# Optimization experiments

Hardware: AMD Instinct MI355X
Metric: run time of the kernel (lower is better)

The kernel has to match this reference:

```python
import jax, jax.numpy as jnp
import numpy as np
import math

S, D = 8192, 128

def setup_inputs() -> dict:
    key = jax.random.key(0)
    kq, kk, kv = jax.random.split(key, 3)
    return {
        "q": jax.random.normal(kq, (S, D), dtype=jnp.float32),
        "k": jax.random.normal(kk, (S, D), dtype=jnp.float32),
        "v": jax.random.normal(kv, (S, D), dtype=jnp.float32),
    }

def reference(q, k, v):
    # scores: [S, S]; scale by sqrt(d) as in the torch module
    scale = 1.0 / math.sqrt(q.shape[1])
    scores = (q @ k.T) * scale
    attn = jax.nn.softmax(scores, axis=-1)
    return attn @ v
```

## Files before the change

### kernel.cpp

```cpp
#include <hip/hip_runtime.h>
#include <hip/hip_bf16.h>

#define SEQ 8192
#define HD 128
#define BM 256
#define BN 64
#define NQT (SEQ / BM)
#define THREADS 512

typedef __bf16 bf16_t;
typedef __bf16 bf16x2 __attribute__((ext_vector_type(2)));
typedef __bf16 bf16x8 __attribute__((ext_vector_type(8)));
typedef float f32x4 __attribute__((ext_vector_type(4)));
typedef float f32x16 __attribute__((ext_vector_type(16)));
typedef unsigned int u32x4 __attribute__((ext_vector_type(4)));

#if __has_builtin(__builtin_amdgcn_exp2f)
__device__ inline float exp2_fast(float x) { return __builtin_amdgcn_exp2f(x); }
#else
__device__ inline float exp2_fast(float x) { return exp2f(x); }
#endif

__device__ inline void permswap32(unsigned int& a, unsigned int& b) {
#if __has_builtin(__builtin_amdgcn_permlane32_swap)
  auto r = __builtin_amdgcn_permlane32_swap(a, b, false, false);
  a = (unsigned int)r[0];
  b = (unsigned int)r[1];
#else
  asm volatile("v_permlane32_swap_b32 %0, %1" : "+v"(a), "+v"(b));
#endif
}

__device__ inline void load_lds16(const void* g, void* l) {
  __builtin_amdgcn_global_load_lds(
      (const __attribute__((address_space(1))) void*)g,
      (__attribute__((address_space(3))) void*)l, 16, 0, 0);
}

__global__ __launch_bounds__(256) void prep_kernel(const float* __restrict__ K,
                                                   const float* __restrict__ V,
                                                   bf16_t* __restrict__ Kb,
                                                   bf16_t* __restrict__ VT) {
  const int b = (int)blockIdx.x;
  const int tid = (int)threadIdx.x;
  if (b < 256) {
    __shared__ float tile[64][65];
    const int T = b & 127;
    const int d0 = (b >> 7) * 64;
    const int s0 = T * 64;
    const int r = tid >> 2;
    const int c0 = (tid & 3) * 16;
#pragma unroll
    for (int j4 = 0; j4 < 4; ++j4) {
      float4 x = *(const float4*)&V[(size_t)(s0 + r) * HD + d0 + c0 + j4 * 4];
      tile[r][c0 + j4 * 4 + 0] = x.x;
      tile[r][c0 + j4 * 4 + 1] = x.y;
      tile[r][c0 + j4 * 4 + 2] = x.z;
      tile[r][c0 + j4 * 4 + 3] = x.w;
    }
    __syncthreads();
    const int d_l = tid & 63;
    const int kc0 = (tid >> 6) * 2;
#pragma unroll
    for (int k2 = 0; k2 < 2; ++k2) {
      const int kc = kc0 + k2;
      bf16x8 wv;
#pragma unroll
      for (int j = 0; j < 8; ++j) wv[j] = (bf16_t)tile[kc * 8 + j][d_l];
      *(bf16x8*)&VT[((size_t)(T * 8 + kc) * 128 + d0 + d_l) * 8] = wv;
    }
  } else {
    const int base = (b - 256) * 2048 + tid * 8;
    const int row = base >> 7;
    const int c = (base >> 3) & 15;
    const int T = row >> 6;
    const int r = row & 63;
    float4 a = *(const float4*)&K[base];
    float4 cc = *(const float4*)&K[base + 4];
    bf16x8 f;
    f[0] = (bf16_t)a.x; f[1] = (bf16_t)a.y; f[2] = (bf16_t)a.z; f[3] = (bf16_t)a.w;
    f[4] = (bf16_t)cc.x; f[5] = (bf16_t)cc.y; f[6] = (bf16_t)cc.z; f[7] = (bf16_t)cc.w;
    *(bf16x8*)&Kb[((size_t)(T * 16 + c) * 64 + r) * 8] = f;
  }
}

__global__ __launch_bounds__(THREADS, 2) void fattn_kernel(
    const float* __restrict__ Q, const bf16_t* __restrict__ Kb,
    const bf16_t* __restrict__ VT, float* __restrict__ Opart,
    float* __restrict__ Lpart, int kshift, int nit) {
  __shared__ __align__(16) bf16_t kt2[2][16][64][8];
  __shared__ __align__(16) bf16_t vt3[3][8][128][8];

  const int tid = (int)threadIdx.x;
  const int lane = tid & 63;
  const int w = tid >> 6;
  const int h = lane >> 5;
  const int n32 = lane & 31;

  const int qt = (int)blockIdx.x >> kshift;
  const int sp = (int)blockIdx.x & ((1 << kshift) - 1);
  const int qbase = qt * BM;
  const int tile0 = sp * nit;

  const float SC2 = 0.08838834764831845f * 1.4426950408889634f;

  bf16x8 qf[8];
  {
    const float* qp = Q + (size_t)(qbase + w * 32 + n32) * HD + h * 8;
#pragma unroll
    for (int kk = 0; kk < 8; ++kk) {
      float4 a = *(const float4*)(qp + kk * 16);
      float4 b = *(const float4*)(qp + kk * 16 + 4);
      bf16x8 f;
      f[0] = (bf16_t)(a.x * SC2); f[1] = (bf16_t)(a.y * SC2);
      f[2] = (bf16_t)(a.z * SC2); f[3] = (bf16_t)(a.w * SC2);
      f[4] = (bf16_t)(b.x * SC2); f[5] = (bf16_t)(b.y * SC2);
      f[6] = (bf16_t)(b.z * SC2); f[7] = (bf16_t)(b.w * SC2);
      qf[kk] = f;
    }
  }

  f32x16 o_acc[4];
#pragma unroll
  for (int i = 0; i < 4; ++i)
#pragma unroll
    for (int e = 0; e < 16; ++e) o_acc[i][e] = 0.f;
  float l_acc = 0.f;

  bf16x8 paA[4], paB[4];

  const int rr0 = w * 2;

#define EXPPACK1(SACC, KK2, PDST_EXPR)                                     \
  {                                                                        \
    float pf[8];                                                           \
    _Pragma("unroll")                                                      \
    for (int j = 0; j < 8; ++j) pf[j] = exp2_fast((SACC)[8 * (KK2) + j]);  \
    l_acc += ((pf[0] + pf[1]) + (pf[2] + pf[3])) +                         \
             ((pf[4] + pf[5]) + (pf[6] + pf[7]));                          \
    bf16x2 p0, p1, p2, p3;                                                 \
    p0[0] = (bf16_t)pf[0]; p0[1] = (bf16_t)pf[1];                          \
    p1[0] = (bf16_t)pf[2]; p1[1] = (bf16_t)pf[3];                          \
    p2[0] = (bf16_t)pf[4]; p2[1] = (bf16_t)pf[5];                          \
    p3[0] = (bf16_t)pf[6]; p3[1] = (bf16_t)pf[7];                          \
    unsigned int sA = __builtin_bit_cast(unsigned int, p0);                \
    unsigned int sB = __builtin_bit_cast(unsigned int, p1);                \
    unsigned int sC = __builtin_bit_cast(unsigned int, p2);                \
    unsigned int sD = __builtin_bit_cast(unsigned int, p3);                \
    permswap32(sA, sC);                                                    \
    permswap32(sB, sD);                                                    \
    u32x4 fv;                                                              \
    fv[0] = sA; fv[1] = sB; fv[2] = sC; fv[3] = sD;                        \
    (PDST_EXPR) = __builtin_bit_cast(bf16x8, fv);                          \
  }

#define PVC(PP, C)                                                         \
  _Pragma("unroll")                                                        \
  for (int ot = 0; ot < 4; ++ot) {                                         \
    bf16x8 vb = *(const bf16x8*)&vt3[vp][(C) * 2 + h][ot * 32 + n32][0];   \
    o_acc[ot] = __builtin_amdgcn_mfma_f32_32x32x16_bf16(PP[C], vb, o_acc[ot], 0, 0, 0); \
  }

#define FBODY(IT, PPREV, PCUR, KC)                                         \
  {                                                                        \
    const int it_ = (IT);                                                  \
    if (it_ + 1 < nit) {                                                   \
      const int ntile = tile0 + it_ + 1;                                   \
      _Pragma("unroll")                                                    \
      for (int t = 0; t < 2; ++t) {                                        \
        const int rr = rr0 + t;                                            \
        load_lds16(Kb + ((size_t)(ntile * 16 + rr) * 64 + lane) * 8,       \
                   (char*)&kt2[(KC) ^ 1][0][0][0] + rr * 1024);            \
        load_lds16(VT + ((size_t)(ntile * 8 + (rr >> 1)) * 128 + (rr & 1) * 64 + lane) * 8, \
                   (char*)&vt3[vd][0][0][0] + rr * 1024);                  \
      }                                                                    \
    }                                                                      \
    f32x16 sacc0, sacc1;                                                   \
    _Pragma("unroll")                                                      \
    for (int e = 0; e < 16; ++e) { sacc0[e] = 0.f; sacc1[e] = 0.f; }       \
    _Pragma("unroll")                                                      \
    for (int kk = 0; kk < 8; ++kk) {                                       \
      bf16x8 af0 = *(const bf16x8*)&kt2[KC][2 * kk + h][n32][0];           \
      sacc0 = __builtin_amdgcn_mfma_f32_32x32x16_bf16(af0, qf[kk], sacc0, 0, 0, 0); \
      bf16x8 af1 = *(const bf16x8*)&kt2[KC][2 * kk + h][32 + n32][0];      \
      sacc1 = __builtin_amdgcn_mfma_f32_32x32x16_bf16(af1, qf[kk], sacc1, 0, 0, 0); \
    }                                                                      \
    PVC(PPREV, 0) EXPPACK1(sacc0, 0, PCUR[0])                              \
    PVC(PPREV, 1) EXPPACK1(sacc0, 1, PCUR[1])                              \
    PVC(PPREV, 2) EXPPACK1(sacc1, 0, PCUR[2])                              \
    PVC(PPREV, 3) EXPPACK1(sacc1, 1, PCUR[3])                              \
    vp = (vp + 1 == 3) ? 0 : vp + 1;                                       \
    vd = (vd + 1 == 3) ? 0 : vd + 1;                                       \
    __syncthreads();                                                       \
  }

#pragma unroll
  for (int t = 0; t < 2; ++t) {
    const int rr = rr0 + t;
    load_lds16(Kb + ((size_t)(tile0 * 16 + rr) * 64 + lane) * 8,
               (char*)&kt2[0][0][0][0] + rr * 1024);
    load_lds16(VT + ((size_t)(tile0 * 8 + (rr >> 1)) * 128 + (rr & 1) * 64 + lane) * 8,
               (char*)&vt3[0][0][0][0] + rr * 1024);
  }
  __syncthreads();

  {
    if (nit > 1) {
      const int ntile = tile0 + 1;
#pragma unroll
      for (int t = 0; t < 2; ++t) {
        const int rr = rr0 + t;
        load_lds16(Kb + ((size_t)(ntile * 16 + rr) * 64 + lane) * 8,
                   (char*)&kt2[1][0][0][0] + rr * 1024);
        load_lds16(VT + ((size_t)(ntile * 8 + (rr >> 1)) * 128 + (rr & 1) * 64 + lane) * 8,
                   (char*)&vt3[1][0][0][0] + rr * 1024);
      }
    }
    f32x16 sacc0, sacc1;
#pragma unroll
    for (int e = 0; e < 16; ++e) { sacc0[e] = 0.f; sacc1[e] = 0.f; }
#pragma unroll
    for (int kk = 0; kk < 8; ++kk) {
      bf16x8 af0 = *(const bf16x8*)&kt2[0][2 * kk + h][n32][0];
      sacc0 = __builtin_amdgcn_mfma_f32_32x32x16_bf16(af0, qf[kk], sacc0, 0, 0, 0);
      bf16x8 af1 = *(const bf16x8*)&kt2[0][2 * kk + h][32 + n32][0];
      sacc1 = __builtin_amdgcn_mfma_f32_32x32x16_bf16(af1, qf[kk], sacc1, 0, 0, 0);
    }
    EXPPACK1(sacc0, 0, paA[0])
    EXPPACK1(sacc0, 1, paA[1])
    EXPPACK1(sacc1, 0, paA[2])
    EXPPACK1(sacc1, 1, paA[3])
    __syncthreads();
  }

  int vp = 0;
  int vd = 2;

  for (int it = 1; it + 1 <= nit - 1; it += 2) {
    FBODY(it, paA, paB, 1)
    FBODY(it + 1, paB, paA, 0)
  }
  FBODY(nit - 1, paA, paB, 1)

#pragma unroll
  for (int C = 0; C < 4; ++C) {
#pragma unroll
    for (int ot = 0; ot < 4; ++ot) {
      bf16x8 vb = *(const bf16x8*)&vt3[vp][C * 2 + h][ot * 32 + n32][0];
      o_acc[ot] = __builtin_amdgcn_mfma_f32_32x32x16_bf16(paB[C], vb, o_acc[ot], 0, 0, 0);
    }
  }

#undef FBODY
#undef PVC
#undef EXPPACK1

  {
    float* op = Opart + ((size_t)sp * SEQ + qbase + w * 32) * HD;
#pragma unroll
    for (int ot = 0; ot < 4; ++ot)
#pragma unroll
      for (int reg = 0; reg < 16; ++reg) {
        const int row = (reg & 3) + 8 * (reg >> 2) + 4 * h;
        op[row * HD + ot * 32 + n32] = o_acc[ot][reg];
      }
    float l = l_acc + __shfl_xor(l_acc, 32);
    if (lane < 32)
      Lpart[(size_t)sp * SEQ + qbase + w * 32 + n32] = l;
  }
}

__global__ __launch_bounds__(256) void combine_kernel(const float* __restrict__ Opart,
                                                      const float* __restrict__ Lpart,
                                                      float* __restrict__ out, int ksplit) {
  const int tid = (int)threadIdx.x;
  const int row = (int)blockIdx.x * 8 + (tid >> 5);
  const int c0 = (tid & 31) * 4;
  float lsum = 0.f;
  for (int s = 0; s < ksplit; ++s) lsum += Lpart[(size_t)s * SEQ + row];
  f32x4 acc;
#pragma unroll
  for (int e = 0; e < 4; ++e) acc[e] = 0.f;
  for (int s = 0; s < ksplit; ++s) {
    f32x4 o = *(const f32x4*)&Opart[((size_t)s * SEQ + row) * HD + c0];
#pragma unroll
    for (int e = 0; e < 4; ++e) acc[e] += o[e];
  }
  const float inv = 1.0f / lsum;
  f32x4 res;
#pragma unroll
  for (int e = 0; e < 4; ++e) res[e] = acc[e] * inv;
  *(f32x4*)&out[(size_t)row * HD + c0] = res;
}

extern "C" void kernel_launch(void* const* d_in, const int* in_sizes, int n_in,
                              void* d_out, int out_size, void* d_ws, size_t ws_size,
                              hipStream_t stream) {
  const float* Q = (const float*)d_in[0];
  const float* K = (const float*)d_in[1];
  const float* V = (const float*)d_in[2];
  float* out = (float*)d_out;

  int ksplit = 8, kshift = 3;
  while (ksplit > 1) {
    size_t need = (size_t)ksplit * SEQ * HD * 4
                + (size_t)ksplit * SEQ * 4
                + (size_t)SEQ * HD * 2 * 2;
    if (need <= ws_size) break;
    ksplit >>= 1; kshift--;
  }

  char* ws = (char*)d_ws;
  float* Opart = (float*)ws;
  float* Lpart = (float*)(ws + (size_t)ksplit * SEQ * HD * 4);
  bf16_t* Kb = (bf16_t*)(ws + (size_t)ksplit * SEQ * HD * 4 + (size_t)ksplit * SEQ * 4);
  bf16_t* VT = Kb + (size_t)SEQ * HD;

  const int nit = SEQ / (ksplit * BN);

  prep_kernel<<<768, 256, 0, stream>>>(K, V, Kb, VT);
  fattn_kernel<<<NQT * ksplit, THREADS, 0, stream>>>(Q, Kb, VT, Opart, Lpart, kshift, nit);
  combine_kernel<<<SEQ / 8, 256, 0, stream>>>(Opart, Lpart, out, ksplit);
}
```

Baseline: 110.8 us.

## Halve attention block threads, each wave computes 64 query rows

Cuts the attention block from 8 waves to 4, and each wave now handles two 32-row query groups. Every K and V fragment read from LDS is therefore reused across two sets of MFMAs, which halves LDS read traffic per FLOP, and each thread issues twice as many async tile loads. The cost is doubled accumulator and Q-fragment registers per thread, with launch bounds relaxed to one block per CU, so occupancy drops and there is a risk of register spills or less latency hiding.

```diff
diff --git a/kernel.cpp b/kernel.cpp
--- a/kernel.cpp
+++ b/kernel.cpp
@@ -6,7 +6,7 @@
 #define BM 256
 #define BN 64
 #define NQT (SEQ / BM)
-#define THREADS 512
+#define THREADS 256
 
 typedef __bf16 bf16_t;
 typedef __bf16 bf16x2 __attribute__((ext_vector_type(2)));
@@ -84,7 +84,7 @@
   }
 }
 
-__global__ __launch_bounds__(THREADS, 2) void fattn_kernel(
+__global__ __launch_bounds__(THREADS, 1) void fattn_kernel(
     const float* __restrict__ Q, const bf16_t* __restrict__ Kb,
     const bf16_t* __restrict__ VT, float* __restrict__ Opart,
     float* __restrict__ Lpart, int kshift, int nit) {
@@ -104,9 +104,10 @@
 
   const float SC2 = 0.08838834764831845f * 1.4426950408889634f;
 
-  bf16x8 qf[8];
-  {
-    const float* qp = Q + (size_t)(qbase + w * 32 + n32) * HD + h * 8;
+  bf16x8 qf[2][8];
+#pragma unroll
+  for (int qg = 0; qg < 2; ++qg) {
+    const float* qp = Q + (size_t)(qbase + w * 64 + qg * 32 + n32) * HD + h * 8;
 #pragma unroll
     for (int kk = 0; kk < 8; ++kk) {
       float4 a = *(const float4*)(qp + kk * 16);
@@ -116,28 +117,30 @@
       f[2] = (bf16_t)(a.z * SC2); f[3] = (bf16_t)(a.w * SC2);
       f[4] = (bf16_t)(b.x * SC2); f[5] = (bf16_t)(b.y * SC2);
       f[6] = (bf16_t)(b.z * SC2); f[7] = (bf16_t)(b.w * SC2);
-      qf[kk] = f;
-    }
-  }
-
-  f32x16 o_acc[4];
-#pragma unroll
-  for (int i = 0; i < 4; ++i)
-#pragma unroll
-    for (int e = 0; e < 16; ++e) o_acc[i][e] = 0.f;
-  float l_acc = 0.f;
-
-  bf16x8 paA[4], paB[4];
-
-  const int rr0 = w * 2;
-
-#define EXPPACK1(SACC, KK2, PDST_EXPR)                                     \
+      qf[qg][kk] = f;
+    }
+  }
+
+  f32x16 o_acc[2][4];
+#pragma unroll
+  for (int qg = 0; qg < 2; ++qg)
+#pragma unroll
+    for (int i = 0; i < 4; ++i)
+#pragma unroll
+      for (int e = 0; e < 16; ++e) o_acc[qg][i][e] = 0.f;
+  float l_acc0 = 0.f, l_acc1 = 0.f;
+
+  bf16x8 paA[2][4], paB[2][4];
+
+  const int rr0 = w * 4;
+
+#define EXPPACK1(SACC, KK2, PDST_EXPR, LACC)                               \
   {                                                                        \
     float pf[8];                                                           \
     _Pragma("unroll")                                                      \
     for (int j = 0; j < 8; ++j) pf[j] = exp2_fast((SACC)[8 * (KK2) + j]);  \
-    l_acc += ((pf[0] + pf[1]) + (pf[2] + pf[3])) +                         \
-             ((pf[4] + pf[5]) + (pf[6] + pf[7]));                          \
+    LACC += ((pf[0] + pf[1]) + (pf[2] + pf[3])) +                          \
+            ((pf[4] + pf[5]) + (pf[6] + pf[7]));                           \
     bf16x2 p0, p1, p2, p3;                                                 \
     p0[0] = (bf16_t)pf[0]; p0[1] = (bf16_t)pf[1];                          \
     p1[0] = (bf16_t)pf[2]; p1[1] = (bf16_t)pf[3];                          \
@@ -154,11 +157,12 @@
     (PDST_EXPR) = __builtin_bit_cast(bf16x8, fv);                          \
   }
 
-#define PVC(PP, C)                                                         \
+#define PVC2(PP, C)                                                        \
   _Pragma("unroll")                                                        \
   for (int ot = 0; ot < 4; ++ot) {                                         \
     bf16x8 vb = *(const bf16x8*)&vt3[vp][(C) * 2 + h][ot * 32 + n32][0];   \
-    o_acc[ot] = __builtin_amdgcn_mfma_f32_32x32x16_bf16(PP[C], vb, o_acc[ot], 0, 0, 0); \
+    o_acc[0][ot] = __builtin_amdgcn_mfma_f32_32x32x16_bf16(PP[0][C], vb, o_acc[0][ot], 0, 0, 0); \
+    o_acc[1][ot] = __builtin_amdgcn_mfma_f32_32x32x16_bf16(PP[1][C], vb, o_acc[1][ot], 0, 0, 0); \
   }
 
 #define FBODY(IT, PPREV, PCUR, KC)                                         \
@@ -167,7 +171,7 @@
     if (it_ + 1 < nit) {                                                   \
       const int ntile = tile0 + it_ + 1;                                   \
       _Pragma("unroll")                                                    \
-      for (int t = 0; t < 2; ++t) {                                        \
+      for (int t = 0; t < 4; ++t) {                                        \
         const int rr = rr0 + t;                                            \
         load_lds16(Kb + ((size_t)(ntile * 16 + rr) * 64 + lane) * 8,       \
                    (char*)&kt2[(KC) ^ 1][0][0][0] + rr * 1024);            \
@@ -175,27 +179,33 @@
                    (char*)&vt3[vd][0][0][0] + rr * 1024);                  \
       }                                                                    \
     }                                                                      \
-    f32x16 sacc0, sacc1;                                                   \
+    f32x16 s00, s10, s01, s11;        \
     _Pragma("unroll")                                                      \
-    for (int e = 0; e < 16; ++e) { sacc0[e] = 0.f; sacc1[e] = 0.f; }       \
+    for (int e = 0; e < 16; ++e) { s00[e] = 0.f; s10[e] = 0.f; s01[e] = 0.f; s11[e] = 0.f; } \
     _Pragma("unroll")                                                      \
     for (int kk = 0; kk < 8; ++kk) {                                       \
       bf16x8 af0 = *(const bf16x8*)&kt2[KC][2 * kk + h][n32][0];           \
-      sacc0 = __builtin_amdgcn_mfma_f32_32x32x16_bf16(af0, qf[kk], sacc0, 0, 0, 0); \
       bf16x8 af1 = *(const bf16x8*)&kt2[KC][2 * kk + h][32 + n32][0];      \
-      sacc1 = __builtin_amdgcn_mfma_f32_32x32x16_bf16(af1, qf[kk], sacc1, 0, 0, 0); \
+      s00 = __builtin_amdgcn_mfma_f32_32x32x16_bf16(af0, qf[0][kk], s00, 0, 0, 0); \
+      s10 = __builtin_amdgcn_mfma_f32_32x32x16_bf16(af1, qf[0][kk], s10, 0, 0, 0); \
+      s01 = __builtin_amdgcn_mfma_f32_32x32x16_bf16(af0, qf[1][kk], s01, 0, 0, 0); \
+      s11 = __builtin_amdgcn_mfma_f32_32x32x16_bf16(af1, qf[1][kk], s11, 0, 0, 0); \
     }                                                                      \
-    PVC(PPREV, 0) EXPPACK1(sacc0, 0, PCUR[0])                              \
-    PVC(PPREV, 1) EXPPACK1(sacc0, 1, PCUR[1])                              \
-    PVC(PPREV, 2) EXPPACK1(sacc1, 0, PCUR[2])                              \
-    PVC(PPREV, 3) EXPPACK1(sacc1, 1, PCUR[3])                              \
+    PVC2(PPREV, 0)                                                         \
+    EXPPACK1(s00, 0, PCUR[0][0], l_acc0) EXPPACK1(s00, 1, PCUR[0][1], l_acc0) \
+    PVC2(PPREV, 1)                                                         \
+    EXPPACK1(s10, 0, PCUR[0][2], l_acc0) EXPPACK1(s10, 1, PCUR[0][3], l_acc0) \
+    PVC2(PPREV, 2)                                                         \
+    EXPPACK1(s01, 0, PCUR[1][0], l_acc1) EXPPACK1(s01, 1, PCUR[1][1], l_acc1) \
+    PVC2(PPREV, 3)                                                         \
+    EXPPACK1(s11, 0, PCUR[1][2], l_acc1) EXPPACK1(s11, 1, PCUR[1][3], l_acc1) \
     vp = (vp + 1 == 3) ? 0 : vp + 1;                                       \
     vd = (vd + 1 == 3) ? 0 : vd + 1;                                       \
     __syncthreads();                                                       \
   }
 
 #pragma unroll
-  for (int t = 0; t < 2; ++t) {
+  for (int t = 0; t < 4; ++t) {
     const int rr = rr0 + t;
     load_lds16(Kb + ((size_t)(tile0 * 16 + rr) * 64 + lane) * 8,
                (char*)&kt2[0][0][0][0] + rr * 1024);
@@ -208,7 +218,7 @@
     if (nit > 1) {
       const int ntile = tile0 + 1;
 #pragma unroll
-      for (int t = 0; t < 2; ++t) {
+      for (int t = 0; t < 4; ++t) {
         const int rr = rr0 + t;
         load_lds16(Kb + ((size_t)(ntile * 16 + rr) * 64 + lane) * 8,
                    (char*)&kt2[1][0][0][0] + rr * 1024);
@@ -216,20 +226,22 @@
                    (char*)&vt3[1][0][0][0] + rr * 1024);
       }
     }
-    f32x16 sacc0, sacc1;
-#pragma unroll
-    for (int e = 0; e < 16; ++e) { sacc0[e] = 0.f; sacc1[e] = 0.f; }
+    f32x16 s00, s10, s01, s11;
+#pragma unroll
+    for (int e = 0; e < 16; ++e) { s00[e] = 0.f; s10[e] = 0.f; s01[e] = 0.f; s11[e] = 0.f; }
 #pragma unroll
     for (int kk = 0; kk < 8; ++kk) {
       bf16x8 af0 = *(const bf16x8*)&kt2[0][2 * kk + h][n32][0];
-      sacc0 = __builtin_amdgcn_mfma_f32_32x32x16_bf16(af0, qf[kk], sacc0, 0, 0, 0);
       bf16x8 af1 = *(const bf16x8*)&kt2[0][2 * kk + h][32 + n32][0];
-      sacc1 = __builtin_amdgcn_mfma_f32_32x32x16_bf16(af1, qf[kk], sacc1, 0, 0, 0);
-    }
-    EXPPACK1(sacc0, 0, paA[0])
-    EXPPACK1(sacc0, 1, paA[1])
-    EXPPACK1(sacc1, 0, paA[2])
-    EXPPACK1(sacc1, 1, paA[3])
+      s00 = __builtin_amdgcn_mfma_f32_32x32x16_bf16(af0, qf[0][kk], s00, 0, 0, 0);
+      s10 = __builtin_amdgcn_mfma_f32_32x32x16_bf16(af1, qf[0][kk], s10, 0, 0, 0);
+      s01 = __builtin_amdgcn_mfma_f32_32x32x16_bf16(af0, qf[1][kk], s01, 0, 0, 0);
+      s11 = __builtin_amdgcn_mfma_f32_32x32x16_bf16(af1, qf[1][kk], s11, 0, 0, 0);
+    }
+    EXPPACK1(s00, 0, paA[0][0], l_acc0) EXPPACK1(s00, 1, paA[0][1], l_acc0)
+    EXPPACK1(s10, 0, paA[0][2], l_acc0) EXPPACK1(s10, 1, paA[0][3], l_acc0)
+    EXPPACK1(s01, 0, paA[1][0], l_acc1) EXPPACK1(s01, 1, paA[1][1], l_acc1)
+    EXPPACK1(s11, 0, paA[1][2], l_acc1) EXPPACK1(s11, 1, paA[1][3], l_acc1)
     __syncthreads();
   }
 
@@ -242,31 +254,32 @@
   }
   FBODY(nit - 1, paA, paB, 1)
 
-#pragma unroll
-  for (int C = 0; C < 4; ++C) {
-#pragma unroll
-    for (int ot = 0; ot < 4; ++ot) {
-      bf16x8 vb = *(const bf16x8*)&vt3[vp][C * 2 + h][ot * 32 + n32][0];
-      o_acc[ot] = __builtin_amdgcn_mfma_f32_32x32x16_bf16(paB[C], vb, o_acc[ot], 0, 0, 0);
-    }
-  }
+  PVC2(paB, 0)
+  PVC2(paB, 1)
+  PVC2(paB, 2)
+  PVC2(paB, 3)
 
 #undef FBODY
-#undef PVC
+#undef PVC2
 #undef EXPPACK1
 
   {
-    float* op = Opart + ((size_t)sp * SEQ + qbase + w * 32) * HD;
-#pragma unroll
-    for (int ot = 0; ot < 4; ++ot)
-#pragma unroll
-      for (int reg = 0; reg < 16; ++reg) {
-        const int row = (reg & 3) + 8 * (reg >> 2) + 4 * h;
-        op[row * HD + ot * 32 + n32] = o_acc[ot][reg];
-      }
-    float l = l_acc + __shfl_xor(l_acc, 32);
-    if (lane < 32)
-      Lpart[(size_t)sp * SEQ + qbase + w * 32 + n32] = l;
+    float* op = Opart + ((size_t)sp * SEQ + qbase + w * 64) * HD;
+#pragma unroll
+    for (int qg = 0; qg < 2; ++qg)
+#pragma unroll
+      for (int ot = 0; ot < 4; ++ot)
+#pragma unroll
+        for (int reg = 0; reg < 16; ++reg) {
+          const int row = qg * 32 + (reg & 3) + 8 * (reg >> 2) + 4 * h;
+          op[row * HD + ot * 32 + n32] = o_acc[qg][ot][reg];
+        }
+    float l0 = l_acc0 + __shfl_xor(l_acc0, 32);
+    float l1 = l_acc1 + __shfl_xor(l_acc1, 32);
+    if (lane < 32) {
+      Lpart[(size_t)sp * SEQ + qbase + w * 64 + n32] = l0;
+      Lpart[(size_t)sp * SEQ + qbase + w * 64 + 32 + n32] = l1;
+    }
   }
 }
 
```

New measurement: 111.5 us. About the same (+0.6%).

## Halve query tile and split KV columns across warp groups via LDS-shared P

Applied to the files above, without the earlier changes.

Reduces the query block from 256 to 128 rows and splits the 8 warps into two groups: each group computes scores for half of the 64-key tile and half of the output head dimension, exchanging the exp'd probabilities through a new LDS buffer instead of keeping them in registers. V buffering goes from triple to double, and the launch bound asks for 4 blocks per CU, aiming at lower register and LDS pressure and higher occupancy. This adds an extra barrier per iteration plus LDS traffic for P, and needs a cross-group reduction of row sums at the end.

```diff
diff --git a/kernel.cpp b/kernel.cpp
--- a/kernel.cpp
+++ b/kernel.cpp
@@ -3,7 +3,7 @@
 
 #define SEQ 8192
 #define HD 128
-#define BM 256
+#define BM 128
 #define BN 64
 #define NQT (SEQ / BM)
 #define THREADS 512
@@ -84,16 +84,19 @@
   }
 }
 
-__global__ __launch_bounds__(THREADS, 2) void fattn_kernel(
+__global__ __launch_bounds__(THREADS, 4) void fattn_kernel(
     const float* __restrict__ Q, const bf16_t* __restrict__ Kb,
     const bf16_t* __restrict__ VT, float* __restrict__ Opart,
     float* __restrict__ Lpart, int kshift, int nit) {
   __shared__ __align__(16) bf16_t kt2[2][16][64][8];
-  __shared__ __align__(16) bf16_t vt3[3][8][128][8];
+  __shared__ __align__(16) bf16_t vt2[2][8][128][8];
+  __shared__ __align__(16) char pbuf[4][4][64][16];
 
   const int tid = (int)threadIdx.x;
   const int lane = tid & 63;
   const int w = tid >> 6;
+  const int qw = w & 3;
+  const int g = w >> 2;
   const int h = lane >> 5;
   const int n32 = lane & 31;
 
@@ -106,7 +109,7 @@
 
   bf16x8 qf[8];
   {
-    const float* qp = Q + (size_t)(qbase + w * 32 + n32) * HD + h * 8;
+    const float* qp = Q + (size_t)(qbase + qw * 32 + n32) * HD + h * 8;
 #pragma unroll
     for (int kk = 0; kk < 8; ++kk) {
       float4 a = *(const float4*)(qp + kk * 16);
@@ -120,18 +123,16 @@
     }
   }
 
-  f32x16 o_acc[4];
-#pragma unroll
-  for (int i = 0; i < 4; ++i)
+  f32x16 o_acc[2];
+#pragma unroll
+  for (int i = 0; i < 2; ++i)
 #pragma unroll
     for (int e = 0; e < 16; ++e) o_acc[i][e] = 0.f;
   float l_acc = 0.f;
 
-  bf16x8 paA[4], paB[4];
-
   const int rr0 = w * 2;
 
-#define EXPPACK1(SACC, KK2, PDST_EXPR)                                     \
+#define EXPPACK1(SACC, KK2)                                                \
   {                                                                        \
     float pf[8];                                                           \
     _Pragma("unroll")                                                      \
@@ -151,17 +152,10 @@
     permswap32(sB, sD);                                                    \
     u32x4 fv;                                                              \
     fv[0] = sA; fv[1] = sB; fv[2] = sC; fv[3] = sD;                        \
-    (PDST_EXPR) = __builtin_bit_cast(bf16x8, fv);                          \
-  }
-
-#define PVC(PP, C)                                                         \
-  _Pragma("unroll")                                                        \
-  for (int ot = 0; ot < 4; ++ot) {                                         \
-    bf16x8 vb = *(const bf16x8*)&vt3[vp][(C) * 2 + h][ot * 32 + n32][0];   \
-    o_acc[ot] = __builtin_amdgcn_mfma_f32_32x32x16_bf16(PP[C], vb, o_acc[ot], 0, 0, 0); \
-  }
-
-#define FBODY(IT, PPREV, PCUR, KC)                                         \
+    *(u32x4*)&pbuf[qw][g * 2 + (KK2)][lane][0] = fv;                       \
+  }
+
+#define FBODY(IT, KC)                                                      \
   {                                                                        \
     const int it_ = (IT);                                                  \
     if (it_ + 1 < nit) {                                                   \
@@ -171,27 +165,38 @@
         const int rr = rr0 + t;                                            \
         load_lds16(Kb + ((size_t)(ntile * 16 + rr) * 64 + lane) * 8,       \
                    (char*)&kt2[(KC) ^ 1][0][0][0] + rr * 1024);            \
-        load_lds16(VT + ((size_t)(ntile * 8 + (rr >> 1)) * 128 + (rr & 1) * 64 + lane) * 8, \
-                   (char*)&vt3[vd][0][0][0] + rr * 1024);                  \
       }                                                                    \
     }                                                                      \
-    f32x16 sacc0, sacc1;                                                   \
+    {                                                                      \
+      const int vtile = tile0 + it_;                                       \
+      _Pragma("unroll")                                                    \
+      for (int t = 0; t < 2; ++t) {                                        \
+        const int rr = rr0 + t;                                            \
+        load_lds16(VT + ((size_t)(vtile * 8 + (rr >> 1)) * 128 + (rr & 1) * 64 + lane) * 8, \
+                   (char*)&vt2[KC][0][0][0] + rr * 1024);                  \
+      }                                                                    \
+    }                                                                      \
+    f32x16 sacc;                                                           \
     _Pragma("unroll")                                                      \
-    for (int e = 0; e < 16; ++e) { sacc0[e] = 0.f; sacc1[e] = 0.f; }       \
+    for (int e = 0; e < 16; ++e) sacc[e] = 0.f;                            \
     _Pragma("unroll")                                                      \
-    for (int kk = 0; kk < 8; ++kk) {                                       \
-      bf16x8 af0 = *(const bf16x8*)&kt2[KC][2 * kk + h][n32][0];           \
-      sacc0 = __builtin_amdgcn_mfma_f32_32x32x16_bf16(af0, qf[kk], sacc0, 0, 0, 0); \
-      bf16x8 af1 = *(const bf16x8*)&kt2[KC][2 * kk + h][32 + n32][0];      \
-      sacc1 = __builtin_amdgcn_mfma_f32_32x32x16_bf16(af1, qf[kk], sacc1, 0, 0, 0); \
+    for (int C = 0; C < 4; ++C) {                                          \
+      bf16x8 af0 = *(const bf16x8*)&kt2[KC][4 * C + h][g * 32 + n32][0];   \
+      sacc = __builtin_amdgcn_mfma_f32_32x32x16_bf16(af0, qf[2 * C], sacc, 0, 0, 0); \
+      bf16x8 af1 = *(const bf16x8*)&kt2[KC][4 * C + 2 + h][g * 32 + n32][0]; \
+      sacc = __builtin_amdgcn_mfma_f32_32x32x16_bf16(af1, qf[2 * C + 1], sacc, 0, 0, 0); \
+      bf16x8 pa = *(const bf16x8*)&pbuf[qw][C][lane][0];                   \
+      bf16x8 vb0 = *(const bf16x8*)&vt2[(KC) ^ 1][C * 2 + h][g * 64 + n32][0]; \
+      o_acc[0] = __builtin_amdgcn_mfma_f32_32x32x16_bf16(pa, vb0, o_acc[0], 0, 0, 0); \
+      bf16x8 vb1 = *(const bf16x8*)&vt2[(KC) ^ 1][C * 2 + h][g * 64 + 32 + n32][0]; \
+      o_acc[1] = __builtin_amdgcn_mfma_f32_32x32x16_bf16(pa, vb1, o_acc[1], 0, 0, 0); \
     }                                                                      \
-    PVC(PPREV, 0) EXPPACK1(sacc0, 0, PCUR[0])                              \
-    PVC(PPREV, 1) EXPPACK1(sacc0, 1, PCUR[1])                              \
-    PVC(PPREV, 2) EXPPACK1(sacc1, 0, PCUR[2])                              \
-    PVC(PPREV, 3) EXPPACK1(sacc1, 1, PCUR[3])                              \
-    vp = (vp + 1 == 3) ? 0 : vp + 1;                                       \
-    vd = (vd + 1 == 3) ? 0 : vd + 1;                                       \
-    __syncthreads();                                                       \
+                      \
+    asm volatile("s_waitcnt lgkmcnt(0)\n\ts_barrier" ::: "memory");        \
+    __builtin_amdgcn_sched_barrier(0);                                     \
+    EXPPACK1(sacc, 0)                                                      \
+    EXPPACK1(sacc, 1)                                                      \
+    __syncthreads();        \
   }
 
 #pragma unroll
@@ -200,7 +205,7 @@
     load_lds16(Kb + ((size_t)(tile0 * 16 + rr) * 64 + lane) * 8,
                (char*)&kt2[0][0][0][0] + rr * 1024);
     load_lds16(VT + ((size_t)(tile0 * 8 + (rr >> 1)) * 128 + (rr & 1) * 64 + lane) * 8,
-               (char*)&vt3[0][0][0][0] + rr * 1024);
+               (char*)&vt2[0][0][0][0] + rr * 1024);
   }
   __syncthreads();
 
@@ -212,61 +217,59 @@
         const int rr = rr0 + t;
         load_lds16(Kb + ((size_t)(ntile * 16 + rr) * 64 + lane) * 8,
                    (char*)&kt2[1][0][0][0] + rr * 1024);
-        load_lds16(VT + ((size_t)(ntile * 8 + (rr >> 1)) * 128 + (rr & 1) * 64 + lane) * 8,
-                   (char*)&vt3[1][0][0][0] + rr * 1024);
       }
     }
-    f32x16 sacc0, sacc1;
-#pragma unroll
-    for (int e = 0; e < 16; ++e) { sacc0[e] = 0.f; sacc1[e] = 0.f; }
+    f32x16 sacc;
+#pragma unroll
+    for (int e = 0; e < 16; ++e) sacc[e] = 0.f;
 #pragma unroll
     for (int kk = 0; kk < 8; ++kk) {
-      bf16x8 af0 = *(const bf16x8*)&kt2[0][2 * kk + h][n32][0];
-      sacc0 = __builtin_amdgcn_mfma_f32_32x32x16_bf16(af0, qf[kk], sacc0, 0, 0, 0);
-      bf16x8 af1 = *(const bf16x8*)&kt2[0][2 * kk + h][32 + n32][0];
-      sacc1 = __builtin_amdgcn_mfma_f32_32x32x16_bf16(af1, qf[kk], sacc1, 0, 0, 0);
-    }
-    EXPPACK1(sacc0, 0, paA[0])
-    EXPPACK1(sacc0, 1, paA[1])
-    EXPPACK1(sacc1, 0, paA[2])
-    EXPPACK1(sacc1, 1, paA[3])
+      bf16x8 af = *(const bf16x8*)&kt2[0][2 * kk + h][g * 32 + n32][0];
+      sacc = __builtin_amdgcn_mfma_f32_32x32x16_bf16(af, qf[kk], sacc, 0, 0, 0);
+    }
+    EXPPACK1(sacc, 0)
+    EXPPACK1(sacc, 1)
     __syncthreads();
   }
 
-  int vp = 0;
-  int vd = 2;
-
   for (int it = 1; it + 1 <= nit - 1; it += 2) {
-    FBODY(it, paA, paB, 1)
-    FBODY(it + 1, paB, paA, 0)
-  }
-  FBODY(nit - 1, paA, paB, 1)
-
-#pragma unroll
-  for (int C = 0; C < 4; ++C) {
-#pragma unroll
-    for (int ot = 0; ot < 4; ++ot) {
-      bf16x8 vb = *(const bf16x8*)&vt3[vp][C * 2 + h][ot * 32 + n32][0];
-      o_acc[ot] = __builtin_amdgcn_mfma_f32_32x32x16_bf16(paB[C], vb, o_acc[ot], 0, 0, 0);
-    }
-  }
+    FBODY(it, 1)
+    FBODY(it + 1, 0)
+  }
+  FBODY(nit - 1, 1)
+
+  {
+    const int vb_buf = (nit - 1) & 1;
+#pragma unroll
+    for (int C = 0; C < 4; ++C) {
+      bf16x8 pa = *(const bf16x8*)&pbuf[qw][C][lane][0];
+      bf16x8 vb0 = *(const bf16x8*)&vt2[vb_buf][C * 2 + h][g * 64 + n32][0];
+      o_acc[0] = __builtin_amdgcn_mfma_f32_32x32x16_bf16(pa, vb0, o_acc[0], 0, 0, 0);
+      bf16x8 vb1 = *(const bf16x8*)&vt2[vb_buf][C * 2 + h][g * 64 + 32 + n32][0];
+      o_acc[1] = __builtin_amdgcn_mfma_f32_32x32x16_bf16(pa, vb1, o_acc[1], 0, 0, 0);
+    }
+  }
+  __syncthreads();
 
 #undef FBODY
-#undef PVC
 #undef EXPPACK1
 
   {
-    float* op = Opart + ((size_t)sp * SEQ + qbase + w * 32) * HD;
-#pragma unroll
-    for (int ot = 0; ot < 4; ++ot)
+    float* op = Opart + ((size_t)sp * SEQ + qbase + qw * 32) * HD + g * 64;
+#pragma unroll
+    for (int ot = 0; ot < 2; ++ot)
 #pragma unroll
       for (int reg = 0; reg < 16; ++reg) {
         const int row = (reg & 3) + 8 * (reg >> 2) + 4 * h;
         op[row * HD + ot * 32 + n32] = o_acc[ot][reg];
       }
     float l = l_acc + __shfl_xor(l_acc, 32);
-    if (lane < 32)
-      Lpart[(size_t)sp * SEQ + qbase + w * 32 + n32] = l;
+    float* lfb = (float*)pbuf;
+    if (lane < 32) lfb[g * 128 + qw * 32 + n32] = l;
+    __syncthreads();
+    if (g == 0 && lane < 32)
+      Lpart[(size_t)sp * SEQ + qbase + qw * 32 + n32] =
+          l + lfb[128 + qw * 32 + n32];
   }
 }
 
```

Result: slower. 133.6 us (+20.5%).

## Triple-buffer K tiles and use partial vmcnt waits at barriers

Applied to the files above, without the earlier changes.

K tiles move from double to triple LDS buffering so that K is prefetched two tiles ahead, while V stays one tile behind its use. The generic __syncthreads is replaced with an explicit s_waitcnt vmcnt(N) plus s_barrier, so each barrier waits only for the older asynchronous global-to-LDS loads and lets newer ones stay in flight. The intent is to hide global load latency behind the MFMA work. In exchange it uses more LDS, which may limit occupancy, and the loop structure now assumes a fixed minimum iteration count (nit of at least 4 or so).

```diff
diff --git a/kernel.cpp b/kernel.cpp
--- a/kernel.cpp
+++ b/kernel.cpp
@@ -36,6 +36,12 @@
       (const __attribute__((address_space(1))) void*)g,
       (__attribute__((address_space(3))) void*)l, 16, 0, 0);
 }
+
+#define BARRIER(N)                                                         \
+  do {                                                                     \
+    asm volatile("s_waitcnt vmcnt(" #N ") lgkmcnt(0)\n\ts_barrier" ::: "memory"); \
+    __builtin_amdgcn_sched_barrier(0);                                     \
+  } while (0)
 
 __global__ __launch_bounds__(256) void prep_kernel(const float* __restrict__ K,
                                                    const float* __restrict__ V,
@@ -88,7 +94,7 @@
     const float* __restrict__ Q, const bf16_t* __restrict__ Kb,
     const bf16_t* __restrict__ VT, float* __restrict__ Opart,
     float* __restrict__ Lpart, int kshift, int nit) {
-  __shared__ __align__(16) bf16_t kt2[2][16][64][8];
+  __shared__ __align__(16) bf16_t kt3[3][16][64][8];
   __shared__ __align__(16) bf16_t vt3[3][8][128][8];
 
   const int tid = (int)threadIdx.x;
@@ -130,6 +136,23 @@
   bf16x8 paA[4], paB[4];
 
   const int rr0 = w * 2;
+  char* const ktB = (char*)&kt3[0][0][0][0];
+  char* const vtB = (char*)&vt3[0][0][0][0];
+
+#define DMA_K(TILE, BUF)                                                   \
+  _Pragma("unroll")                                                        \
+  for (int t = 0; t < 2; ++t) {                                            \
+    const int rr = rr0 + t;                                                \
+    load_lds16(Kb + ((size_t)((TILE) * 16 + rr) * 64 + lane) * 8,          \
+               ktB + (BUF) * 16384 + rr * 1024);                           \
+  }
+#define DMA_V(TILE, BUF)                                                   \
+  _Pragma("unroll")                                                        \
+  for (int t = 0; t < 2; ++t) {                                            \
+    const int rr = rr0 + t;                                                \
+    load_lds16(VT + ((size_t)((TILE) * 8 + (rr >> 1)) * 128 + (rr & 1) * 64 + lane) * 8, \
+               vtB + (BUF) * 16384 + rr * 1024);                           \
+  }
 
 #define EXPPACK1(SACC, KK2, PDST_EXPR)                                     \
   {                                                                        \
@@ -157,103 +180,85 @@
 #define PVC(PP, C)                                                         \
   _Pragma("unroll")                                                        \
   for (int ot = 0; ot < 4; ++ot) {                                         \
-    bf16x8 vb = *(const bf16x8*)&vt3[vp][(C) * 2 + h][ot * 32 + n32][0];   \
+    bf16x8 vb = *(const bf16x8*)(vtB + vp * 16384 + ((C) * 2 + h) * 2048 + \
+                                 (ot * 32 + n32) * 16);                    \
     o_acc[ot] = __builtin_amdgcn_mfma_f32_32x32x16_bf16(PP[C], vb, o_acc[ot], 0, 0, 0); \
   }
 
-#define FBODY(IT, PPREV, PCUR, KC)                                         \
+#define FBODY(PPREV, PCUR, DOK, DOV, VMN)                                  \
   {                                                                        \
-    const int it_ = (IT);                                                  \
-    if (it_ + 1 < nit) {                                                   \
-      const int ntile = tile0 + it_ + 1;                                   \
-      _Pragma("unroll")                                                    \
-      for (int t = 0; t < 2; ++t) {                                        \
-        const int rr = rr0 + t;                                            \
-        load_lds16(Kb + ((size_t)(ntile * 16 + rr) * 64 + lane) * 8,       \
-                   (char*)&kt2[(KC) ^ 1][0][0][0] + rr * 1024);            \
-        load_lds16(VT + ((size_t)(ntile * 8 + (rr >> 1)) * 128 + (rr & 1) * 64 + lane) * 8, \
-                   (char*)&vt3[vd][0][0][0] + rr * 1024);                  \
-      }                                                                    \
-    }                                                                      \
+    if (DOK) { DMA_K(ktile, kd) }                                          \
+    if (DOV) { DMA_V(vtile, vd) }                                          \
     f32x16 sacc0, sacc1;                                                   \
     _Pragma("unroll")                                                      \
     for (int e = 0; e < 16; ++e) { sacc0[e] = 0.f; sacc1[e] = 0.f; }       \
     _Pragma("unroll")                                                      \
     for (int kk = 0; kk < 8; ++kk) {                                       \
-      bf16x8 af0 = *(const bf16x8*)&kt2[KC][2 * kk + h][n32][0];           \
+      bf16x8 af0 = *(const bf16x8*)(ktB + kc * 16384 + (2 * kk + h) * 1024 + n32 * 16); \
       sacc0 = __builtin_amdgcn_mfma_f32_32x32x16_bf16(af0, qf[kk], sacc0, 0, 0, 0); \
-      bf16x8 af1 = *(const bf16x8*)&kt2[KC][2 * kk + h][32 + n32][0];      \
+      bf16x8 af1 = *(const bf16x8*)(ktB + kc * 16384 + (2 * kk + h) * 1024 + (32 + n32) * 16); \
       sacc1 = __builtin_amdgcn_mfma_f32_32x32x16_bf16(af1, qf[kk], sacc1, 0, 0, 0); \
     }                                                                      \
     PVC(PPREV, 0) EXPPACK1(sacc0, 0, PCUR[0])                              \
     PVC(PPREV, 1) EXPPACK1(sacc0, 1, PCUR[1])                              \
     PVC(PPREV, 2) EXPPACK1(sacc1, 0, PCUR[2])                              \
     PVC(PPREV, 3) EXPPACK1(sacc1, 1, PCUR[3])                              \
+    BARRIER(VMN);                                                          \
+    kc = (kc + 1 == 3) ? 0 : kc + 1;                                       \
+    kd = (kd + 1 == 3) ? 0 : kd + 1;                                       \
     vp = (vp + 1 == 3) ? 0 : vp + 1;                                       \
     vd = (vd + 1 == 3) ? 0 : vd + 1;                                       \
-    __syncthreads();                                                       \
-  }
-
-#pragma unroll
-  for (int t = 0; t < 2; ++t) {
-    const int rr = rr0 + t;
-    load_lds16(Kb + ((size_t)(tile0 * 16 + rr) * 64 + lane) * 8,
-               (char*)&kt2[0][0][0][0] + rr * 1024);
-    load_lds16(VT + ((size_t)(tile0 * 8 + (rr >> 1)) * 128 + (rr & 1) * 64 + lane) * 8,
-               (char*)&vt3[0][0][0][0] + rr * 1024);
-  }
-  __syncthreads();
+    ++ktile; ++vtile;                                                      \
+  }
+
+  DMA_K(tile0, 0)
+  DMA_V(tile0, 0)
+  DMA_K(tile0 + 1, 1)
+  BARRIER(2);
 
   {
-    if (nit > 1) {
-      const int ntile = tile0 + 1;
-#pragma unroll
-      for (int t = 0; t < 2; ++t) {
-        const int rr = rr0 + t;
-        load_lds16(Kb + ((size_t)(ntile * 16 + rr) * 64 + lane) * 8,
-                   (char*)&kt2[1][0][0][0] + rr * 1024);
-        load_lds16(VT + ((size_t)(ntile * 8 + (rr >> 1)) * 128 + (rr & 1) * 64 + lane) * 8,
-                   (char*)&vt3[1][0][0][0] + rr * 1024);
-      }
-    }
+    DMA_K(tile0 + 2, 2)
+    DMA_V(tile0 + 1, 1)
     f32x16 sacc0, sacc1;
 #pragma unroll
     for (int e = 0; e < 16; ++e) { sacc0[e] = 0.f; sacc1[e] = 0.f; }
 #pragma unroll
     for (int kk = 0; kk < 8; ++kk) {
-      bf16x8 af0 = *(const bf16x8*)&kt2[0][2 * kk + h][n32][0];
+      bf16x8 af0 = *(const bf16x8*)(ktB + (2 * kk + h) * 1024 + n32 * 16);
       sacc0 = __builtin_amdgcn_mfma_f32_32x32x16_bf16(af0, qf[kk], sacc0, 0, 0, 0);
-      bf16x8 af1 = *(const bf16x8*)&kt2[0][2 * kk + h][32 + n32][0];
+      bf16x8 af1 = *(const bf16x8*)(ktB + (2 * kk + h) * 1024 + (32 + n32) * 16);
       sacc1 = __builtin_amdgcn_mfma_f32_32x32x16_bf16(af1, qf[kk], sacc1, 0, 0, 0);
     }
     EXPPACK1(sacc0, 0, paA[0])
     EXPPACK1(sacc0, 1, paA[1])
     EXPPACK1(sacc1, 0, paA[2])
     EXPPACK1(sacc1, 1, paA[3])
-    __syncthreads();
-  }
-
-  int vp = 0;
-  int vd = 2;
-
-  for (int it = 1; it + 1 <= nit - 1; it += 2) {
-    FBODY(it, paA, paB, 1)
-    FBODY(it + 1, paB, paA, 0)
-  }
-  FBODY(nit - 1, paA, paB, 1)
-
-#pragma unroll
-  for (int C = 0; C < 4; ++C) {
-#pragma unroll
-    for (int ot = 0; ot < 4; ++ot) {
-      bf16x8 vb = *(const bf16x8*)&vt3[vp][C * 2 + h][ot * 32 + n32][0];
-      o_acc[ot] = __builtin_amdgcn_mfma_f32_32x32x16_bf16(paB[C], vb, o_acc[ot], 0, 0, 0);
-    }
-  }
+    BARRIER(4);
+  }
+
+  int kc = 1, kd = 0;
+  int vp = 0, vd = 2;
+  int ktile = tile0 + 3;
+  int vtile = tile0 + 2;
+
+  for (int it = 1; it <= nit - 4; it += 2) {
+    FBODY(paA, paB, 1, 1, 4)
+    FBODY(paB, paA, 1, 1, 4)
+  }
+  FBODY(paA, paB, 1, 1, 4)
+  FBODY(paB, paA, 0, 1, 2)
+  FBODY(paA, paB, 0, 0, 0)
+
+  PVC(paB, 0)
+  PVC(paB, 1)
+  PVC(paB, 2)
+  PVC(paB, 3)
 
 #undef FBODY
 #undef PVC
 #undef EXPPACK1
+#undef DMA_K
+#undef DMA_V
 
   {
     float* op = Opart + ((size_t)sp * SEQ + qbase + w * 32) * HD;
```

Result: no change. 110.7 us (-0.1%).
